# Kernel optimization log

Hardware: AMD Instinct MI355X
Metric: run time of the kernel (lower is better)

Reference implementation:

```python
import jax, jax.numpy as jnp
import numpy as np

N_QUBITS = 8
N_LAYERS = 2
BATCH = 16384
INPUT_DIM = 3072
NUM_CLASSES = 10

I2 = np.eye(2, dtype=np.complex64)
PAULIS = [
    I2,
    np.array([[0, 1], [1, 0]], np.complex64),      # X
    np.array([[0, -1j], [1j, 0]], np.complex64),   # Y
    np.array([[1, 0], [0, -1]], np.complex64),     # Z
]
XX = np.kron(PAULIS[1], PAULIS[1])
YY = np.kron(PAULIS[2], PAULIS[2])
ZZ = np.kron(PAULIS[3], PAULIS[3])
I4 = np.eye(4, dtype=np.complex64)


def u3(p):
    # PennyLane U3(theta, phi, lambda)
    th, ph, lam = p[0], p[1], p[2]
    c = jnp.cos(th / 2).astype(jnp.complex64)
    s = jnp.sin(th / 2).astype(jnp.complex64)
    return jnp.stack([
        jnp.stack([c, -jnp.exp(1j * lam) * s]),
        jnp.stack([jnp.exp(1j * ph) * s, jnp.exp(1j * (ph + lam)) * c]),
    ])


def cu3(p):
    U = u3(p)
    Z = jnp.zeros((2, 2), U.dtype)
    Ic = jnp.asarray(I2)
    top = jnp.concatenate([Ic, Z], axis=1)
    bot = jnp.concatenate([Z, U], axis=1)
    return jnp.concatenate([top, bot], axis=0)


def ising(P, phi):
    # exp(-i phi/2 * P) with P a 2-qubit Pauli word (P^2 = I)
    return jnp.cos(phi / 2) * I4 - 1j * jnp.sin(phi / 2) * P


def apply_1q(psi, U, w):
    psi = jnp.moveaxis(psi, 1 + w, -1)
    psi = jnp.einsum('ij,...j->...i', U, psi)
    return jnp.moveaxis(psi, -1, 1 + w)


def apply_2q(psi, U, a, b):
    psi = jnp.moveaxis(psi, (1 + a, 1 + b), (-2, -1))
    sh = psi.shape
    psi = jnp.einsum('ij,...j->...i', U, psi.reshape(sh[:-2] + (4,)))
    return jnp.moveaxis(psi.reshape(sh), (-2, -1), (1 + a, 1 + b))


def apply_ry_batched(psi, theta, w):
    # per-sample RY angle (AngleEmbedding, rotation='Y')
    c = jnp.cos(theta / 2).reshape((-1,) + (1,) * (psi.ndim - 2))
    s = jnp.sin(theta / 2).reshape((-1,) + (1,) * (psi.ndim - 2))
    psi = jnp.moveaxis(psi, 1 + w, -1)
    a0, a1 = psi[..., 0], psi[..., 1]
    psi = jnp.stack([c * a0 - s * a1, s * a0 + c * a1], axis=-1)
    return jnp.moveaxis(psi, -1, 1 + w)


def dilated_conv(psi, W, wires):
    n = len(wires)
    if n == 8:
        pairs = [(0, 2), (1, 3), (4, 6), (5, 7)]
    elif n == 4:
        pairs = [(0, 2), (1, 3)]
    elif n == 2:
        pairs = [(0, 1)]
    else:
        pairs = [(i, i + 2) for i in range(n - 2)]
    processed = set()
    for q1, q2 in pairs:
        if q1 in wires and q2 in wires:
            psi = apply_1q(psi, u3(W[q1, 0:3]), q1)
            psi = apply_1q(psi, u3(W[q2, 3:6]), q2)
            psi = apply_2q(psi, ising(ZZ, W[q1, 6]), q1, q2)
            psi = apply_2q(psi, ising(YY, W[q1, 7]), q1, q2)
            psi = apply_2q(psi, ising(XX, W[q1, 8]), q1, q2)
            psi = apply_1q(psi, u3(W[q1, 9:12]), q1)
            psi = apply_1q(psi, u3(W[q2, 12:15]), q2)
            processed.update((q1, q2))
    for w in wires:
        if w not in processed:
            for i in range(5):
                psi = apply_1q(psi, u3(W[w, 3 * i:3 * i + 3]), w)
    return psi


def pooling(psi, P, wires):
    for indx, w in enumerate(wires):
        if indx % 2 == 1:
            # measure wire w, cond-U3 on wires[indx-1]; deferred -> CU3(ctrl=w, tgt=wires[indx-1])
            psi = apply_2q(psi, cu3(P[indx // 2]), w, wires[indx - 1])
    return psi


def _gray_pauli_words(k):
    # matches pennylane _n_k_gray_code(4, k) ordering, identity word dropped
    words = []
    for i in range(4 ** k):
        br = []
        v = i
        for _ in range(k):
            br.append(v % 4)
            v //= 4
        cw = [0] * k
        shift = 0
        for j in reversed(range(k)):
            cw[j] = (br[j] + shift) % 4
            shift += 4 - cw[j]
        if any(cw):
            words.append(tuple(cw))
    return words


def arbitrary_unitary(psi, weights, wires):
    # qml.ArbitraryUnitary: sequence of PauliRot(weights[i], word) gates
    k = len(wires)
    Ik = np.eye(2 ** k, dtype=np.complex64)
    for idx, cw in enumerate(_gray_pauli_words(k)):
        P = np.array([[1.0]], np.complex64)
        for p in cw:
            P = np.kron(P, PAULIS[p])
        th = weights[idx]
        G = jnp.cos(th / 2) * Ik - 1j * jnp.sin(th / 2) * P
        psi = apply_2q(psi, G, wires[0], wires[1])
    return psi


def run_circuit(features, conv, pool, last):
    B = features.shape[0]
    psi = jnp.zeros((B, 2 ** N_QUBITS), jnp.complex64).at[:, 0].set(1.0)
    psi = psi.reshape((B,) + (2,) * N_QUBITS)
    for w in range(N_QUBITS):
        psi = apply_ry_batched(psi, features[:, w], w)
    wires = list(range(N_QUBITS))
    for layer in range(N_LAYERS):
        psi = dilated_conv(psi, conv[layer], wires)
        psi = pooling(psi, pool[layer], wires)
        wires = wires[::2]
    psi = arbitrary_unitary(psi, last, wires)
    probs = psi.real ** 2 + psi.imag ** 2
    z0 = probs[:, 0].reshape(B, -1).sum(-1) - probs[:, 1].reshape(B, -1).sum(-1)
    return z0  # <Z_0> per sample


def setup_inputs():
    key = jax.random.key(0)
    ks = jax.random.split(key, 8)
    return {
        'x': jax.random.normal(ks[0], (BATCH, INPUT_DIM), jnp.float32),
        'fc_w': jax.random.normal(ks[1], (N_QUBITS, INPUT_DIM), jnp.float32) * 0.02,
        'fc_b': jnp.zeros((N_QUBITS,), jnp.float32),
        'conv_params': jax.random.normal(ks[2], (N_LAYERS, N_QUBITS, 15), jnp.float32),
        'pool_params': jax.random.normal(ks[3], (N_LAYERS, N_QUBITS // 2, 3), jnp.float32),
        'last_params': jax.random.normal(ks[4], (15,), jnp.float32),
        'fc_out_w': jax.random.normal(ks[5], (NUM_CLASSES, 1), jnp.float32),
        'fc_out_b': jnp.zeros((NUM_CLASSES,), jnp.float32),
    }


def reference(x, fc_w, fc_b, conv_params, pool_params, last_params, fc_out_w, fc_out_b):
    reduced = jnp.tanh(x @ fc_w.T + fc_b)                      # (B, n_qubits)
    z0 = run_circuit(reduced, conv_params, pool_params, last_params)  # (B,)
    logits = z0[:, None] * fc_out_w[:, 0][None, :] + fc_out_b  # (B, num_classes)
    return logits
```

## Files before the change

### kernel.cpp

```cpp
#include <hip/hip_runtime.h>
#include <math.h>

__device__ inline float2 cmul(float2 a, float2 b){
  return make_float2(a.x*b.x - a.y*b.y, a.x*b.y + a.y*b.x);
}

__device__ inline void mk_u3(const float* p, float2& u00, float2& u01, float2& u10, float2& u11){
  float s, c;   sincosf(0.5f*p[0], &s, &c);
  float sl, cl; sincosf(p[1], &sl, &cl);
  float sm, cm; sincosf(p[2], &sm, &cm);
  float s2, c2; sincosf(p[1] + p[2], &s2, &c2);
  u00 = make_float2(c, 0.f);
  u01 = make_float2(-s*cm, -s*sm);
  u10 = make_float2( s*cl,  s*sl);
  u11 = make_float2( c*c2,  c*s2);
}

__device__ inline void pauli2(int t, float2* m){
  if (t == 0){ m[0]=make_float2(1,0); m[1]=make_float2(0,0);  m[2]=make_float2(0,0); m[3]=make_float2(1,0); }
  else if (t == 1){ m[0]=make_float2(0,0); m[1]=make_float2(1,0);  m[2]=make_float2(1,0); m[3]=make_float2(0,0); }
  else if (t == 2){ m[0]=make_float2(0,0); m[1]=make_float2(0,-1); m[2]=make_float2(0,1); m[3]=make_float2(0,0); }
  else            { m[0]=make_float2(1,0); m[1]=make_float2(0,0);  m[2]=make_float2(0,0); m[3]=make_float2(-1,0);}
}

struct GSpec { int type; int w1; int w2; int poff; };
#define NG 66
__device__ const GSpec gspec[NG] = {
  {0,0,0,  0},{0,2,0, 33},{1,0,2,  6},{2,0,2,  7},{3,0,2,  8},{0,0,0,  9},{0,2,0, 42},
  {0,1,0, 15},{0,3,0, 48},{1,1,3, 21},{2,1,3, 22},{3,1,3, 23},{0,1,0, 24},{0,3,0, 57},
  {0,4,0, 60},{0,6,0, 93},{1,4,6, 66},{2,4,6, 67},{3,4,6, 68},{0,4,0, 69},{0,6,0,102},
  {0,5,0, 75},{0,7,0,108},{1,5,7, 81},{2,5,7, 82},{3,5,7, 83},{0,5,0, 84},{0,7,0,117},
  {4,1,0,1000},{4,3,2,1003},{4,5,4,1006},{4,7,6,1009},
  {0,0,0,120},{0,2,0,153},{1,0,2,126},{2,0,2,127},{3,0,2,128},{0,0,0,129},{0,2,0,162},
  {0,4,0,180},{0,4,0,183},{0,4,0,186},{0,4,0,189},{0,4,0,192},
  {0,6,0,210},{0,6,0,213},{0,6,0,216},{0,6,0,219},{0,6,0,222},
  {4,2,0,1012},{4,6,4,1015},
  {5,1,0,2000},{5,2,0,2001},{5,3,0,2002},{5,3,1,2003},{5,0,1,2004},
  {5,1,1,2005},{5,2,1,2006},{5,2,2,2007},{5,3,2,2008},{5,0,2,2009},
  {5,1,2,2010},{5,1,3,2011},{5,2,3,2012},{5,3,3,2013},{5,0,3,2014},
};

__device__ inline void apply1q(float2* S, int lane, int bit,
                               float2 u00, float2 u01, float2 u10, float2 u11){
  #pragma unroll
  for (int t = 0; t < 2; t++){
    int p  = lane + 64*t;
    int k0 = ((p >> bit) << (bit+1)) | (p & ((1<<bit)-1));
    int k1 = k0 | (1 << bit);
    float2 a = S[k0], b = S[k1];
    float2 na = make_float2(u00.x*a.x - u00.y*a.y + u01.x*b.x - u01.y*b.y,
                            u00.x*a.y + u00.y*a.x + u01.x*b.y + u01.y*b.x);
    float2 nb = make_float2(u10.x*a.x - u10.y*a.y + u11.x*b.x - u11.y*b.y,
                            u10.x*a.y + u10.y*a.x + u11.x*b.y + u11.y*b.x);
    S[k0] = na; S[k1] = nb;
  }
  __syncthreads();
}

__device__ inline void apply2q(float2* S, int lane, int bitA, int bitB, const float2* G){
  int hi = bitA > bitB ? bitA : bitB;
  int lo = bitA ^ bitB ^ hi;
  int t2  = ((lane >> lo) << (lo+1)) | (lane & ((1<<lo)-1));
  int k00 = ((t2   >> hi) << (hi+1)) | (t2   & ((1<<hi)-1));
  int mA = 1 << bitA, mB = 1 << bitB;
  int id[4] = { k00, k00|mB, k00|mA, k00|mA|mB };
  float2 v[4];
  #pragma unroll
  for (int r = 0; r < 4; r++) v[r] = S[id[r]];
  #pragma unroll
  for (int r = 0; r < 4; r++){
    float re = 0.f, im = 0.f;
    #pragma unroll
    for (int c = 0; c < 4; c++){
      float2 g = G[r*4 + c];
      re += g.x*v[c].x - g.y*v[c].y;
      im += g.x*v[c].y + g.y*v[c].x;
    }
    S[id[r]] = make_float2(re, im);
  }
  __syncthreads();
}

__global__ __launch_bounds__(64) void kern_sim(const float* __restrict__ conv,
                                               const float* __restrict__ pool,
                                               const float* __restrict__ last,
                                               float2* __restrict__ U){
  __shared__ float2 Gt[NG*16];
  __shared__ float2 S[256];
  const int lane = threadIdx.x;
  const int j = blockIdx.x;

  for (int g = lane; g < NG; g += 64){
    GSpec sp = gspec[g];
    const float* base;
    if (sp.poff >= 2000)      base = last + (sp.poff - 2000);
    else if (sp.poff >= 1000) base = pool + (sp.poff - 1000);
    else                      base = conv + sp.poff;
    float2 G[16];
    #pragma unroll
    for (int i = 0; i < 16; i++) G[i] = make_float2(0.f, 0.f);
    if (sp.type == 0){
      float2 a,b,c,d; mk_u3(base,a,b,c,d);
      G[0]=a; G[1]=b; G[2]=c; G[3]=d;
    } else if (sp.type == 1){
      float s,co; sincosf(0.5f*base[0], &s, &co);
      G[0]=make_float2(co,-s); G[5]=make_float2(co,s); G[10]=make_float2(co,s); G[15]=make_float2(co,-s);
    } else if (sp.type == 2){
      float s,co; sincosf(0.5f*base[0], &s, &co);
      G[0]=G[5]=G[10]=G[15]=make_float2(co,0.f);
      G[3]=make_float2(0.f,s); G[6]=make_float2(0.f,-s); G[9]=make_float2(0.f,-s); G[12]=make_float2(0.f,s);
    } else if (sp.type == 3){
      float s,co; sincosf(0.5f*base[0], &s, &co);
      G[0]=G[5]=G[10]=G[15]=make_float2(co,0.f);
      G[3]=G[6]=G[9]=G[12]=make_float2(0.f,-s);
    } else if (sp.type == 4){
      float2 a,b,c,d; mk_u3(base,a,b,c,d);
      G[0]=make_float2(1.f,0.f); G[5]=make_float2(1.f,0.f);
      G[10]=a; G[11]=b; G[14]=c; G[15]=d;
    } else {
      float s,co; sincosf(0.5f*base[0], &s, &co);
      float2 A2[4], B2[4]; pauli2(sp.w1,A2); pauli2(sp.w2,B2);
      #pragma unroll
      for (int i1 = 0; i1 < 2; i1++)
      #pragma unroll
      for (int i2 = 0; i2 < 2; i2++)
      #pragma unroll
      for (int j1 = 0; j1 < 2; j1++)
      #pragma unroll
      for (int j2 = 0; j2 < 2; j2++){
        float2 Pv = cmul(A2[i1*2+j1], B2[i2*2+j2]);
        int rr = i1*2+i2, cc = j1*2+j2;
        G[rr*4+cc] = make_float2((rr==cc ? co : 0.f) + s*Pv.y, -s*Pv.x);
      }
    }
    #pragma unroll
    for (int i = 0; i < 16; i++) Gt[g*16 + i] = G[i];
  }
  #pragma unroll
  for (int t = 0; t < 4; t++){ int k = lane + 64*t; S[k] = make_float2(k==j ? 1.f : 0.f, 0.f); }
  __syncthreads();

  for (int g = 0; g < NG; g++){
    GSpec sp = gspec[g];
    if (sp.type == 0){
      float2 a = Gt[g*16+0], b = Gt[g*16+1], c = Gt[g*16+2], d = Gt[g*16+3];
      apply1q(S, lane, 7 - sp.w1, a, b, c, d);
    } else {
      int bA, bB;
      if (sp.type == 5){ bA = 7; bB = 3; }
      else             { bA = 7 - sp.w1; bB = 7 - sp.w2; }
      apply2q(S, lane, bA, bB, &Gt[g*16]);
    }
  }
  #pragma unroll
  for (int t = 0; t < 4; t++){ int k = lane + 64*t; U[k*256 + j] = S[k]; }
}

__global__ __launch_bounds__(256) void kern_m2(const float2* __restrict__ U,
                                               float* __restrict__ mt){
  __shared__ float dsh[256];
  const int xm = blockIdx.x, i = threadIdx.x;
  const int j2 = i ^ xm;
  float acc = 0.f;
  #pragma unroll 4
  for (int k = 0; k < 128; k++){
    float2 ui0 = U[k*256 + i];
    float2 uj0 = U[k*256 + j2];
    float2 ui1 = U[(k+128)*256 + i];
    float2 uj1 = U[(k+128)*256 + j2];
    acc += (ui0.x*uj0.x + ui0.y*uj0.y) - (ui1.x*uj1.x + ui1.y*uj1.y);
  }
  dsh[i] = acc;
  __syncthreads();
  for (int bit = 1; bit < 256; bit <<= 1){
    float mine = dsh[i], other = dsh[i ^ bit];
    __syncthreads();
    dsh[i] = (i & bit) ? (other - mine) : (mine + other);
    __syncthreads();
  }
  if ((i & xm) == 0){
    int idx = 0, pw = 1;
    #pragma unroll
    for (int b2 = 0; b2 < 8; b2++){
      int dg = ((xm >> b2) & 1) ? 1 : (((i >> b2) & 1) ? 2 : 0);
      idx += dg * pw; pw *= 3;
    }
    mt[idx] = dsh[i] * (1.0f/256.0f);
  }
}

__global__ __launch_bounds__(256) void kern_gemv(const float* __restrict__ x,
                                                 const float* __restrict__ w,
                                                 const float* __restrict__ b,
                                                 float* __restrict__ red){
  __shared__ float4 wl[3072];
  const int tid = threadIdx.x;
  const int wave = tid >> 6, lane = tid & 63;
  const int rl = lane >> 5, co = lane & 31;
  const int row = blockIdx.x*8 + wave*2 + rl;
  const float4* xp = (const float4*)(x + (size_t)row*3072);
  const float4* wp = (const float4*)w;
  float acc[8];
  #pragma unroll
  for (int q = 0; q < 8; q++) acc[q] = 0.f;

  #pragma unroll
  for (int half = 0; half < 2; half++){
    __syncthreads();
    #pragma unroll
    for (int i = 0; i < 12; i++){
      int idx = tid + 256*i;
      int q = idx / 384, cc = idx - q*384;
      wl[idx] = wp[q*768 + half*384 + cc];
    }
    __syncthreads();
    #pragma unroll 2
    for (int it = 0; it < 12; it++){
      int cl = it*32 + co;
      float4 xv = xp[half*384 + cl];
      #pragma unroll
      for (int q = 0; q < 8; q++){
        float4 wv = wl[q*384 + cl];
        acc[q] += wv.x*xv.x + wv.y*xv.y + wv.z*xv.z + wv.w*xv.w;
      }
    }
  }

  #pragma unroll
  for (int q = 0; q < 8; q++){
    float v = acc[q];
    v += __shfl_xor(v, 1);
    v += __shfl_xor(v, 2);
    v += __shfl_xor(v, 4);
    v += __shfl_xor(v, 8);
    v += __shfl_xor(v, 16);
    acc[q] = v;
  }
  if (co == 0){
    float4 o0 = make_float4(tanhf(acc[0]+b[0]), tanhf(acc[1]+b[1]),
                            tanhf(acc[2]+b[2]), tanhf(acc[3]+b[3]));
    float4 o1 = make_float4(tanhf(acc[4]+b[4]), tanhf(acc[5]+b[5]),
                            tanhf(acc[6]+b[6]), tanhf(acc[7]+b[7]));
    float4* rp = (float4*)(red + (size_t)row*8);
    rp[0] = o0; rp[1] = o1;
  }
}

__global__ __launch_bounds__(256) void kern_contract(const float* __restrict__ red,
                                                     const float* __restrict__ mt,
                                                     const float* __restrict__ fow,
                                                     const float* __restrict__ fob,
                                                     float* __restrict__ out){
  __shared__ float mtl[9*27*32];
  __shared__ float zsh[4*64];
  const int tid = threadIdx.x;
  for (int idx = tid; idx < 9*27*32; idx += 256){
    int h  = idx / 864;
    int r  = idx - h*864;
    int mm = r >> 5, l = r & 31;
    mtl[idx] = (l < 27) ? mt[h*729 + mm*27 + l] : 0.f;
  }
  const int wave = tid >> 6, lane = tid & 63;
  const int e = blockIdx.x*64 + lane;
  const float4* rp = (const float4*)(red + (size_t)e*8);
  float4 r0 = rp[0], r1 = rp[1];
  __syncthreads();

  float rr[8] = {r0.x, r0.y, r0.z, r0.w, r1.x, r1.y, r1.z, r1.w};
  float sn[8], cs[8];
  #pragma unroll
  for (int q = 0; q < 8; q++) sincosf(rr[q], &sn[q], &cs[q]);
  float f0[3] = {1.f, sn[7], cs[7]};
  float f1[3] = {1.f, sn[6], cs[6]};
  float f2[3] = {1.f, sn[5], cs[5]};
  float g27[32];
  #pragma unroll
  for (int z = 27; z < 32; z++) g27[z] = 0.f;
  #pragma unroll
  for (int d2 = 0; d2 < 3; d2++)
  #pragma unroll
  for (int d1 = 0; d1 < 3; d1++)
  #pragma unroll
  for (int d0 = 0; d0 < 3; d0++)
    g27[9*d2 + 3*d1 + d0] = f2[d2]*f1[d1]*f0[d0];
  float4 glo4[8];
  #pragma unroll
  for (int v = 0; v < 8; v++)
    glo4[v] = make_float4(g27[4*v], g27[4*v+1], g27[4*v+2], g27[4*v+3]);
  float f3[3] = {1.f, sn[4], cs[4]};
  float f4[3] = {1.f, sn[3], cs[3]};
  float f5[3] = {1.f, sn[2], cs[2]};
  float gmid[27];
  #pragma unroll
  for (int d5 = 0; d5 < 3; d5++)
  #pragma unroll
  for (int d4 = 0; d4 < 3; d4++)
  #pragma unroll
  for (int d3 = 0; d3 < 3; d3++)
    gmid[9*d5 + 3*d4 + d3] = f5[d5]*f4[d4]*f3[d3];
  float f6[3] = {1.f, sn[1], cs[1]};
  float f7[3] = {1.f, sn[0], cs[0]};
  float ghi[9];
  #pragma unroll
  for (int d7 = 0; d7 < 3; d7++)
  #pragma unroll
  for (int d6 = 0; d6 < 3; d6++)
    ghi[3*d7 + d6] = f7[d7]*f6[d6];

  const int hbeg = (wave==0) ? 0 : (wave==1) ? 3 : (wave==2) ? 5 : 7;
  const int hend = hbeg + ((wave==0) ? 3 : 2);
  float part = 0.f;
  for (int h = hbeg; h < hend; h++){
    float ha = 0.f, hb = 0.f;
    #pragma unroll 3
    for (int mm = 0; mm < 27; mm++){
      const float4* mp = (const float4*)&mtl[(h*27 + mm) << 5];
      float d0 = 0.f, d1 = 0.f;
      #pragma unroll
      for (int v = 0; v < 8; v += 2){
        float4 m0 = mp[v], m1 = mp[v+1];
        d0 += m0.x*glo4[v].x   + m0.y*glo4[v].y   + m0.z*glo4[v].z   + m0.w*glo4[v].w;
        d1 += m1.x*glo4[v+1].x + m1.y*glo4[v+1].y + m1.z*glo4[v+1].z + m1.w*glo4[v+1].w;
      }
      float term = (d0 + d1) * gmid[mm];
      if (mm & 1) hb += term; else ha += term;
    }
    part += (ha + hb) * ghi[h];
  }
  zsh[wave*64 + lane] = part;
  __syncthreads();

  for (int idx = tid; idx < 640; idx += 256){
    int el = idx / 10, c = idx - el*10;
    float z = zsh[el] + zsh[64+el] + zsh[128+el] + zsh[192+el];
    out[((size_t)blockIdx.x*64 + el)*10 + c] = z*fow[c] + fob[c];
  }
}

extern "C" void kernel_launch(void* const* d_in, const int* in_sizes, int n_in,
                              void* d_out, int out_size, void* d_ws, size_t ws_size,
                              hipStream_t stream) {
  (void)in_sizes; (void)n_in; (void)out_size; (void)ws_size;
  const float* x    = (const float*)d_in[0];
  const float* fcw  = (const float*)d_in[1];
  const float* fcb  = (const float*)d_in[2];
  const float* conv = (const float*)d_in[3];
  const float* pool = (const float*)d_in[4];
  const float* last = (const float*)d_in[5];
  const float* fow  = (const float*)d_in[6];
  const float* fob  = (const float*)d_in[7];
  float* out = (float*)d_out;

  char* ws = (char*)d_ws;
  float2* U   = (float2*)ws;
  float*  red = (float*) (ws + 512*1024);
  float*  mt  = (float*) (ws + 1024*1024);

  kern_sim     <<<256,  64,  0, stream>>>(conv, pool, last, U);
  kern_m2      <<<256,  256, 0, stream>>>(U, mt);
  kern_gemv    <<<2048, 256, 0, stream>>>(x, fcw, fcb, red);
  kern_contract<<<256,  256, 0, stream>>>(red, mt, fow, fob, out);
}
```

Before: 372.8 us.

## Pre-fuse circuit gates into composite 2q unitaries and process two rows per GEMV thread

The simulation kernel now multiplies consecutive gates on the same wire pairs into 14 composite unitaries in shared memory before applying them. This cuts the number of state-vector passes and barriers from the full gate list down to a few fused applications. The GEMV kernel now gives each thread two input rows, halves the shared weight tile, and launches half as many blocks, so each weight load from LDS is reused twice. The cost is more registers per thread and hard-coded gate indices that depend on the circuit layout.

Result: faster. 355.8 us (-4.6%).

```diff
diff --git a/kernel.cpp b/kernel.cpp
--- a/kernel.cpp
+++ b/kernel.cpp
@@ -3,6 +3,10 @@
 
 __device__ inline float2 cmul(float2 a, float2 b){
   return make_float2(a.x*b.x - a.y*b.y, a.x*b.y + a.y*b.x);
+}
+__device__ inline void cfma(float2& acc, float2 a, float2 b){
+  acc.x += a.x*b.x - a.y*b.y;
+  acc.y += a.x*b.y + a.y*b.x;
 }
 
 __device__ inline void mk_u3(const float* p, float2& u00, float2& u01, float2& u10, float2& u11){
@@ -86,6 +90,8 @@
                                                const float* __restrict__ last,
                                                float2* __restrict__ U){
   __shared__ float2 Gt[NG*16];
+  __shared__ float2 Ft[14*16];
+  __shared__ float2 Ms[7*16];
   __shared__ float2 S[256];
   const int lane = threadIdx.x;
   const int j = blockIdx.x;
@@ -136,22 +142,118 @@
     #pragma unroll
     for (int i = 0; i < 16; i++) Gt[g*16 + i] = G[i];
   }
+  __syncthreads();
+
+  const int fe = lane & 15;
+  const int fr = fe >> 2, fc = fe & 3;
+
+  {
+    const int p  = lane >> 4;
+    const int gb = p*7;
+    float2 va = Gt[gb*16     + (fr>>1)*2 + (fc>>1)];
+    float2 vb = Gt[(gb+1)*16 + (fr&1)*2  + (fc&1)];
+    Ms[p*16 + fe] = cmul(va, vb);
+    __syncthreads();
+    for (int s = 0; s < 3; s++){
+      float2 acc = make_float2(0.f, 0.f);
+      #pragma unroll
+      for (int k = 0; k < 4; k++)
+        cfma(acc, Gt[(gb+2+s)*16 + fr*4 + k], Ms[p*16 + k*4 + fc]);
+      __syncthreads();
+      Ms[p*16 + fe] = acc;
+      __syncthreads();
+    }
+    float2 ka = Gt[(gb+5)*16 + (fr>>1)*2 + (fc>>1)];
+    float2 kb = Gt[(gb+6)*16 + (fr&1)*2  + (fc&1)];
+    Ft[p*16 + fe] = cmul(ka, kb);
+    __syncthreads();
+    float2 acc = make_float2(0.f, 0.f);
+    #pragma unroll
+    for (int k = 0; k < 4; k++)
+      cfma(acc, Ft[p*16 + fr*4 + k], Ms[p*16 + k*4 + fc]);
+    __syncthreads();
+    Ft[p*16 + fe] = acc;
+    __syncthreads();
+  }
+
+  {
+    const int grp = lane >> 4;
+    if (grp == 0){
+      float2 va = Gt[32*16 + (fr>>1)*2 + (fc>>1)];
+      float2 vb = Gt[33*16 + (fr&1)*2  + (fc&1)];
+      Ms[4*16 + fe] = cmul(va, vb);
+    } else if (grp == 1){
+      Ms[5*16 + fe] = Gt[51*16 + fe];
+    } else if (lane < 40){
+      int t = (lane-32)>>2, e2 = (lane-32)&3;
+      Ms[6*16 + t*4 + e2] = Gt[(39+5*t)*16 + e2];
+    }
+    __syncthreads();
+    for (int s = 1; s <= 14; s++){
+      float2 val = make_float2(0.f, 0.f);
+      int wf = 0, dst = 0;
+      if (grp == 0){
+        if (s <= 3){
+          #pragma unroll
+          for (int k = 0; k < 4; k++)
+            cfma(val, Gt[(33+s)*16 + fr*4 + k], Ms[4*16 + k*4 + fc]);
+          wf = 1; dst = 4*16 + fe;
+        } else if (s == 4){
+          float2 ka = Gt[37*16 + (fr>>1)*2 + (fc>>1)];
+          float2 kb = Gt[38*16 + (fr&1)*2  + (fc&1)];
+          val = cmul(ka, kb); wf = 1; dst = 0*16 + fe;
+        } else if (s == 5){
+          #pragma unroll
+          for (int k = 0; k < 4; k++)
+            cfma(val, Ms[0*16 + fr*4 + k], Ms[4*16 + k*4 + fc]);
+          wf = 2; dst = 4*16 + fe;
+        }
+      } else if (grp == 1){
+        #pragma unroll
+        for (int k = 0; k < 4; k++)
+          cfma(val, Gt[(51+s)*16 + fr*4 + k], Ms[5*16 + k*4 + fc]);
+        if (s == 14){ wf = 2; dst = 13*16 + fe; }
+        else        { wf = 1; dst = 5*16 + fe; }
+      } else if (lane < 40 && s <= 4){
+        int t = (lane-32)>>2, e2 = (lane-32)&3, r2 = e2>>1, c2 = e2&1;
+        #pragma unroll
+        for (int k = 0; k < 2; k++)
+          cfma(val, Gt[(39+5*t+s)*16 + r2*2 + k], Ms[6*16 + t*4 + k*2 + c2]);
+        if (s == 4){ wf = 2; dst = (5+t)*16 + e2; }
+        else       { wf = 1; dst = 6*16 + t*4 + e2; }
+      }
+      __syncthreads();
+      if (wf == 1) Ms[dst] = val;
+      else if (wf == 2) Ft[dst] = val;
+      __syncthreads();
+    }
+    for (int idx = lane; idx < 96; idx += 64){
+      int q = idx >> 4, e = idx & 15;
+      int gid = (q < 4) ? (28+q) : (q == 4 ? 49 : 50);
+      Ft[(7+q)*16 + e] = Gt[gid*16 + e];
+    }
+  }
+  __syncthreads();
+
   #pragma unroll
   for (int t = 0; t < 4; t++){ int k = lane + 64*t; S[k] = make_float2(k==j ? 1.f : 0.f, 0.f); }
   __syncthreads();
 
-  for (int g = 0; g < NG; g++){
-    GSpec sp = gspec[g];
-    if (sp.type == 0){
-      float2 a = Gt[g*16+0], b = Gt[g*16+1], c = Gt[g*16+2], d = Gt[g*16+3];
-      apply1q(S, lane, 7 - sp.w1, a, b, c, d);
-    } else {
-      int bA, bB;
-      if (sp.type == 5){ bA = 7; bB = 3; }
-      else             { bA = 7 - sp.w1; bB = 7 - sp.w2; }
-      apply2q(S, lane, bA, bB, &Gt[g*16]);
-    }
-  }
+  apply2q(S, lane, 7, 5, &Ft[0*16]);
+  apply2q(S, lane, 6, 4, &Ft[1*16]);
+  apply2q(S, lane, 3, 1, &Ft[2*16]);
+  apply2q(S, lane, 2, 0, &Ft[3*16]);
+  apply2q(S, lane, 6, 7, &Ft[7*16]);
+  apply2q(S, lane, 4, 5, &Ft[8*16]);
+  apply2q(S, lane, 2, 3, &Ft[9*16]);
+  apply2q(S, lane, 0, 1, &Ft[10*16]);
+  apply2q(S, lane, 7, 5, &Ft[4*16]);
+  apply1q(S, lane, 3, Ft[5*16+0], Ft[5*16+1], Ft[5*16+2], Ft[5*16+3]);
+  apply1q(S, lane, 1, Ft[6*16+0], Ft[6*16+1], Ft[6*16+2], Ft[6*16+3]);
+  apply2q(S, lane, 5, 7, &Ft[11*16]);
+  apply2q(S, lane, 1, 3, &Ft[12*16]);
+  apply2q(S, lane, 7, 3, &Ft[13*16]);
+
   #pragma unroll
   for (int t = 0; t < 4; t++){ int k = lane + 64*t; U[k*256 + j] = S[k]; }
 }
@@ -193,56 +295,64 @@
                                                  const float* __restrict__ w,
                                                  const float* __restrict__ b,
                                                  float* __restrict__ red){
-  __shared__ float4 wl[3072];
+  __shared__ float4 wl[1536];
   const int tid = threadIdx.x;
   const int wave = tid >> 6, lane = tid & 63;
   const int rl = lane >> 5, co = lane & 31;
-  const int row = blockIdx.x*8 + wave*2 + rl;
-  const float4* xp = (const float4*)(x + (size_t)row*3072);
-  const float4* wp = (const float4*)w;
-  float acc[8];
-  #pragma unroll
-  for (int q = 0; q < 8; q++) acc[q] = 0.f;
-
-  #pragma unroll
-  for (int half = 0; half < 2; half++){
-    __syncthreads();
-    #pragma unroll
-    for (int i = 0; i < 12; i++){
+  const int row0 = blockIdx.x*16 + wave*4 + rl*2;
+  const float4* xp0 = (const float4*)(x + (size_t)row0*3072);
+  const float4* xp1 = (const float4*)(x + (size_t)(row0+1)*3072);
+  const float4* wp  = (const float4*)w;
+  float accA[8], accB[8];
+  #pragma unroll
+  for (int q = 0; q < 8; q++){ accA[q] = 0.f; accB[q] = 0.f; }
+
+  for (int qt = 0; qt < 4; qt++){
+    __syncthreads();
+    #pragma unroll
+    for (int i = 0; i < 6; i++){
       int idx = tid + 256*i;
-      int q = idx / 384, cc = idx - q*384;
-      wl[idx] = wp[q*768 + half*384 + cc];
-    }
-    __syncthreads();
-    #pragma unroll 2
-    for (int it = 0; it < 12; it++){
+      int q = idx / 192, cc = idx - q*192;
+      wl[idx] = wp[q*768 + qt*192 + cc];
+    }
+    __syncthreads();
+    #pragma unroll
+    for (int it = 0; it < 6; it++){
       int cl = it*32 + co;
-      float4 xv = xp[half*384 + cl];
+      float4 xa = xp0[qt*192 + cl];
+      float4 xb = xp1[qt*192 + cl];
       #pragma unroll
       for (int q = 0; q < 8; q++){
-        float4 wv = wl[q*384 + cl];
-        acc[q] += wv.x*xv.x + wv.y*xv.y + wv.z*xv.z + wv.w*xv.w;
+        float4 wv = wl[q*192 + cl];
+        accA[q] += wv.x*xa.x + wv.y*xa.y + wv.z*xa.z + wv.w*xa.w;
+        accB[q] += wv.x*xb.x + wv.y*xb.y + wv.z*xb.z + wv.w*xb.w;
       }
     }
   }
 
   #pragma unroll
   for (int q = 0; q < 8; q++){
-    float v = acc[q];
-    v += __shfl_xor(v, 1);
-    v += __shfl_xor(v, 2);
-    v += __shfl_xor(v, 4);
-    v += __shfl_xor(v, 8);
-    v += __shfl_xor(v, 16);
-    acc[q] = v;
+    float va = accA[q], vb = accB[q];
+    va += __shfl_xor(va, 1);  vb += __shfl_xor(vb, 1);
+    va += __shfl_xor(va, 2);  vb += __shfl_xor(vb, 2);
+    va += __shfl_xor(va, 4);  vb += __shfl_xor(vb, 4);
+    va += __shfl_xor(va, 8);  vb += __shfl_xor(vb, 8);
+    va += __shfl_xor(va, 16); vb += __shfl_xor(vb, 16);
+    accA[q] = va; accB[q] = vb;
   }
   if (co == 0){
-    float4 o0 = make_float4(tanhf(acc[0]+b[0]), tanhf(acc[1]+b[1]),
-                            tanhf(acc[2]+b[2]), tanhf(acc[3]+b[3]));
-    float4 o1 = make_float4(tanhf(acc[4]+b[4]), tanhf(acc[5]+b[5]),
-                            tanhf(acc[6]+b[6]), tanhf(acc[7]+b[7]));
-    float4* rp = (float4*)(red + (size_t)row*8);
-    rp[0] = o0; rp[1] = o1;
+    float4 a0 = make_float4(tanhf(accA[0]+b[0]), tanhf(accA[1]+b[1]),
+                            tanhf(accA[2]+b[2]), tanhf(accA[3]+b[3]));
+    float4 a1 = make_float4(tanhf(accA[4]+b[4]), tanhf(accA[5]+b[5]),
+                            tanhf(accA[6]+b[6]), tanhf(accA[7]+b[7]));
+    float4* rpA = (float4*)(red + (size_t)row0*8);
+    rpA[0] = a0; rpA[1] = a1;
+    float4 b0 = make_float4(tanhf(accB[0]+b[0]), tanhf(accB[1]+b[1]),
+                            tanhf(accB[2]+b[2]), tanhf(accB[3]+b[3]));
+    float4 b1 = make_float4(tanhf(accB[4]+b[4]), tanhf(accB[5]+b[5]),
+                            tanhf(accB[6]+b[6]), tanhf(accB[7]+b[7]));
+    float4* rpB = (float4*)(red + (size_t)(row0+1)*8);
+    rpB[0] = b0; rpB[1] = b1;
   }
 }
 
@@ -358,6 +468,6 @@
 
   kern_sim     <<<256,  64,  0, stream>>>(conv, pool, last, U);
   kern_m2      <<<256,  256, 0, stream>>>(U, mt);
-  kern_gemv    <<<2048, 256, 0, stream>>>(x, fcw, fcb, red);
+  kern_gemv    <<<1024, 256, 0, stream>>>(x, fcw, fcb, red);
   kern_contract<<<256,  256, 0, stream>>>(red, mt, fow, fob, out);
 }
```
